# Performance work log

Measured on AMD Instinct MI355X. Metric: run time of the kernel, lower is better.

Reference implementation:

```python
import jax, jax.numpy as jnp
import numpy as np

B, C, H, W = 64, 3, 512, 512
KSIZE = 13
EPS = 8.0
IDENTITY_OFFSET = 4.0
DEFORM_OFFSET = (2.0 + IDENTITY_OFFSET / (W - 1)) / 2.0
SCALE_X = IDENTITY_OFFSET / (W - 1)
SCALE_Y = IDENTITY_OFFSET / (H - 1)


def setup_inputs() -> dict:
    key = jax.random.key(0)
    k1, k2 = jax.random.split(key)
    image = jax.random.uniform(k1, (B, C, H, W), dtype=jnp.float32)
    prim_grid = jax.random.normal(k2, (B, 2, H, W), dtype=jnp.float32) * 0.01
    return {"image": image, "prim_grid": prim_grid}


def _samp_iden():
    seq = jnp.arange(-(W - 1), W, 2, dtype=jnp.float32) / (W - 1)
    gx = jnp.broadcast_to(seq[None, :], (H, W))
    gy = gx.T
    return jnp.stack([gx, gy], axis=0)[None]  # [1,2,H,W]


def _gaussian_blur(x, ksize):
    sigma = ksize * 0.15 + 0.35
    half = (ksize - 1) * 0.5
    t = jnp.linspace(-half, half, ksize)
    pdf = jnp.exp(-0.5 * (t / sigma) ** 2)
    k1 = pdf / pdf.sum()
    k2d = jnp.outer(k1, k1)
    p = ksize // 2
    xp = jnp.pad(x, ((0, 0), (0, 0), (p, p), (p, p)), mode='reflect')
    kernel = jnp.broadcast_to(k2d[None, None], (2, 1, ksize, ksize))
    return jax.lax.conv_general_dilated(
        xp, kernel, window_strides=(1, 1), padding='VALID',
        feature_group_count=2, dimension_numbers=('NCHW', 'OIHW', 'NCHW'))


def _samp2accu(samp):
    # conv_transpose with [1,-1] kernel + crop == first-difference with zero prepend
    s = samp + DEFORM_OFFSET
    ax = jnp.diff(s[:, 0:1], axis=3, prepend=jnp.zeros_like(s[:, 0:1, :, :1])) / SCALE_X
    ay = jnp.diff(s[:, 1:2], axis=2, prepend=jnp.zeros_like(s[:, 1:2, :1, :])) / SCALE_Y
    return jnp.concatenate([ax, ay], axis=1)


def _accu2samp(accu):
    # conv_transpose with full-ones kernel + crop == cumulative sum
    sx = jnp.cumsum(accu[:, 0:1] * SCALE_X, axis=3)
    sy = jnp.cumsum(accu[:, 1:2] * SCALE_Y, axis=2)
    return jnp.concatenate([sx, sy], axis=1) - DEFORM_OFFSET


def _grid_sample(image, grid):
    # image [B,C,H,W], grid [B,H,W,2] xy in [-1,1], bilinear, align_corners=True, zeros pad
    gx = (grid[..., 0] + 1.0) * 0.5 * (W - 1)
    gy = (grid[..., 1] + 1.0) * 0.5 * (H - 1)
    x0 = jnp.floor(gx)
    y0 = jnp.floor(gy)
    wx = gx - x0
    wy = gy - y0
    x0i = x0.astype(jnp.int32)
    x1i = x0i + 1
    y0i = y0.astype(jnp.int32)
    y1i = y0i + 1

    def gather(img, yi, xi):
        valid = ((xi >= 0) & (xi < W) & (yi >= 0) & (yi < H)).astype(img.dtype)
        xc = jnp.clip(xi, 0, W - 1)
        yc = jnp.clip(yi, 0, H - 1)
        return img[:, yc, xc] * valid[None]  # [C,H,W]

    def per_b(img, y0i, y1i, x0i, x1i, wx, wy):
        v00 = gather(img, y0i, x0i)
        v01 = gather(img, y0i, x1i)
        v10 = gather(img, y1i, x0i)
        v11 = gather(img, y1i, x1i)
        return (v00 * (1 - wx) * (1 - wy) + v01 * wx * (1 - wy)
                + v10 * (1 - wx) * wy + v11 * wx * wy)

    return jax.vmap(per_b)(image, y0i, y1i, x0i, x1i, wx, wy)


def _forward_grid(prim_grid):
    iden = _samp_iden()
    p = _gaussian_blur(prim_grid, KSIZE)
    accu = jnp.maximum(_samp2accu(p + iden), 0.0)          # accu_clip (relu)
    p = _accu2samp(accu) - iden
    bound = (2.0 / W) * EPS
    p = jnp.clip(p, -bound, bound)                          # prim_clip
    samp = jnp.clip(p + iden, -1.0, 1.0)                    # samp_clip (hardtanh)
    return samp


def reference(image, prim_grid):
    samp = _forward_grid(prim_grid)
    grid = jnp.transpose(samp, (0, 2, 3, 1))  # [B,H,W,2]
    return _grid_sample(image, grid)
```

## Files before the change

kernel.cpp:

```cpp
#include <hip/hip_runtime.h>
#include <math.h>

#define HH 512
#define WW 512
#define NB 64
#define HW (HH*WW)

struct GaussK { float k[13]; };

__device__ __forceinline__ float idenv(int i) {
    return (float)(2*i - (WW-1)) / (float)(WW-1);
}

#define DEF_OFF ((float)((2.0 + 4.0/511.0)/2.0))
#define BOUND   ((float)(2.0/512.0*8.0))

typedef float vf2 __attribute__((ext_vector_type(2), aligned(4)));

__device__ __forceinline__ void hconv_row(const float (&a)[8], int lane, const GaussK& gk, float (&o)[8]) {
    float win[20];
    #pragma unroll
    for (int i = 0; i < 6; ++i) {
        float v = __shfl_up(a[i+2], 1, 64);
        win[i] = (lane == 0) ? a[6-i] : v;
    }
    #pragma unroll
    for (int i = 6; i < 14; ++i) win[i] = a[i-6];
    #pragma unroll
    for (int i = 14; i < 20; ++i) {
        float v = __shfl_down(a[i-14], 1, 64);
        win[i] = (lane == 63) ? a[20-i] : v;
    }
    #pragma unroll
    for (int j = 0; j < 8; ++j) {
        float acc = 0.f;
        #pragma unroll
        for (int i = 0; i < 13; ++i) acc = fmaf(gk.k[i], win[j+i], acc);
        o[j] = acc;
    }
}

__device__ __forceinline__ void xscan_row(const float (&a)[8], int lane, const GaussK& gk, float* row0) {
    float win[21];
    #pragma unroll
    for (int i = 0; i < 7; ++i) {
        float v = __shfl_up(a[i+1], 1, 64);
        win[i] = (lane == 0) ? a[7-i] : v;
    }
    #pragma unroll
    for (int i = 0; i < 8; ++i) win[7+i] = a[i];
    #pragma unroll
    for (int i = 15; i < 21; ++i) {
        float v = __shfl_down(a[i-15], 1, 64);
        win[i] = (lane == 63) ? a[21-i] : v;
    }
    float s[9];
    #pragma unroll
    for (int j = 0; j < 9; ++j) {
        float acc = 0.f;
        #pragma unroll
        for (int i = 0; i < 13; ++i) acc = fmaf(gk.k[i], win[j+i], acc);
        s[j] = acc + idenv(8*lane - 1 + j) + DEF_OFF;
    }
    if (lane == 0) s[0] = 0.f;

    float qs[8], q = 0.f;
    #pragma unroll
    for (int j = 1; j < 9; ++j) { q += fmaxf(s[j] - s[j-1], 0.f); qs[j-1] = q; }
    float inc = q;
    #pragma unroll
    for (int d = 1; d < 64; d <<= 1) {
        float t = __shfl_up(inc, d, 64);
        if (lane >= d) inc += t;
    }
    float excl = inc - q;

    float4 g0, g1;
    float* gp0 = (float*)&g0;
    float* gp1 = (float*)&g1;
    #pragma unroll
    for (int j = 0; j < 8; ++j) {
        int wcol = lane*8 + j;
        float sx = excl + qs[j];
        float p = sx - DEF_OFF - idenv(wcol);
        p = fminf(fmaxf(p, -BOUND), BOUND);
        float g = p + idenv(wcol);
        g = fminf(fmaxf(g, -1.f), 1.f);
        if (j < 4) gp0[j] = g; else gp1[j-4] = g;
    }
    *(float4*)(row0 + lane*8)     = g0;
    *(float4*)(row0 + lane*8 + 4) = g1;
}

__global__ void __launch_bounds__(256) k_prep(const float* __restrict__ prim, float* __restrict__ out, GaussK gk) {
    int lane = threadIdx.x & 63;
    int bid  = (int)blockIdx.x;
    int work = (bid & 7)*256 + (bid >> 3);
    int gw   = work*4 + ((int)threadIdx.x >> 6);
    int b    = gw >> 7;
    int h0   = (gw & 127)*4;

    const float4* src0 = (const float4*)(prim + (size_t)b*2*HW);
    const float*  src1 = prim + ((size_t)b*2 + 1)*HW;
    float* plane0 = out + (size_t)b*3*HW;
    float* plane1 = out + ((size_t)b*3 + 1)*HW;

    float a[4][8];
    #pragma unroll
    for (int r = 0; r < 4; ++r)
        #pragma unroll
        for (int j = 0; j < 8; ++j) a[r][j] = 0.f;

    #pragma unroll
    for (int i = 0; i < 16; ++i) {
        int rr = h0 - 6 + i;
        rr = rr < 0 ? -rr : (rr > HH-1 ? 2*(HH-1) - rr : rr);
        float4 u0 = src0[(size_t)rr*128 + 2*lane];
        float4 u1 = src0[(size_t)rr*128 + 2*lane + 1];
        float vv[8] = {u0.x,u0.y,u0.z,u0.w,u1.x,u1.y,u1.z,u1.w};
        #pragma unroll
        for (int r = 0; r < 4; ++r) {
            if (i >= r && i <= r + 12) {
                #pragma unroll
                for (int j = 0; j < 8; ++j) a[r][j] = fmaf(gk.k[i-r], vv[j], a[r][j]);
            }
        }
    }

    #pragma unroll
    for (int r = 0; r < 4; ++r) {
        const float4* c4 = (const float4*)(src1 + (size_t)(h0+r)*WW);
        float4 u0 = c4[2*lane];
        float4 u1 = c4[2*lane + 1];
        float c[8] = {u0.x,u0.y,u0.z,u0.w,u1.x,u1.y,u1.z,u1.w};
        float o[8];
        hconv_row(c, lane, gk, o);
        float* row1 = plane1 + (size_t)(h0+r)*WW;
        *(float4*)(row1 + lane*8)     = make_float4(o[0],o[1],o[2],o[3]);
        *(float4*)(row1 + lane*8 + 4) = make_float4(o[4],o[5],o[6],o[7]);
    }

    #pragma unroll
    for (int r = 0; r < 4; ++r)
        xscan_row(a[r], lane, gk, plane0 + (size_t)(h0+r)*WW);
}

__global__ void __launch_bounds__(1024, 1) k_yssamp(const float* __restrict__ image, float* __restrict__ out, GaussK gk) {
    __shared__ float segsum[16][64];
    int bid  = (int)blockIdx.x;
    int work = (bid & 7)*64 + (bid >> 3);
    int b    = work >> 3;
    int wt   = work & 7;
    int lane = threadIdx.x & 63;
    int ws   = threadIdx.x >> 6;
    int w    = wt*64 + lane;
    const float* p1 = out + ((size_t)b*3 + 1)*HW + w;
    int r0 = ws*32;

    float v[45];
    #pragma unroll
    for (int j = 0; j < 45; ++j) {
        int r = r0 - 7 + j;
        r = r < 0 ? -r : (r > HH-1 ? 2*(HH-1) - r : r);
        v[j] = p1[(size_t)r*WW];
    }

    float sprev;
    if (ws == 0) {
        sprev = 0.f;
    } else {
        float acc = 0.f;
        #pragma unroll
        for (int i = 0; i < 13; ++i) acc = fmaf(gk.k[i], v[i], acc);
        sprev = acc + idenv(r0 - 1) + DEF_OFF;
    }

    float q[32];
    float run = 0.f;
    #pragma unroll
    for (int n = 0; n < 32; ++n) {
        float acc = 0.f;
        #pragma unroll
        for (int i = 0; i < 13; ++i) acc = fmaf(gk.k[i], v[n+1+i], acc);
        float s = acc + idenv(r0 + n) + DEF_OFF;
        run += fmaxf(s - sprev, 0.f);
        q[n] = run;
        sprev = s;
    }
    segsum[ws][lane] = run;
    __syncthreads();
    float off = 0.f;
    for (int k = 0; k < ws; ++k) off += segsum[k][lane];

    const float* ib = image + (size_t)b*3*HW;
    float*       ob = out   + (size_t)b*3*HW;

    float gxv[32];
    #pragma unroll
    for (int n = 0; n < 32; ++n)
        gxv[n] = ob[(size_t)(r0 + n)*WW + w];

    #pragma unroll
    for (int n = 0; n < 32; ++n) {
        int h = r0 + n;
        size_t poff = (size_t)h*WW + w;
        float p = off + q[n] - DEF_OFF - idenv(h);
        p = fminf(fmaxf(p, -BOUND), BOUND);
        float gy = p + idenv(h);
        gy = fminf(fmaxf(gy, -1.f), 1.f);
        float gx = gxv[n];

        float fx = (gx + 1.f) * 0.5f * (float)(WW-1);
        float fy = (gy + 1.f) * 0.5f * (float)(HH-1);
        float x0f = floorf(fx), y0f = floorf(fy);
        float wx = fx - x0f, wy = fy - y0f;
        int x0 = (int)x0f, y0 = (int)y0f;
        int y1 = y0 + 1; if (y1 > HH-1) y1 = HH-1;
        bool shx = x0 > WW-2;
        int xb = shx ? WW-2 : x0;
        size_t g0 = (size_t)y0*WW + xb;
        size_t g1 = (size_t)y1*WW + xb;
        float w11 = wx*wy;
        float w01 = wx - w11;
        float w10 = wy - w11;
        float w00 = 1.f - wx - wy + w11;
        #pragma unroll
        for (int c = 0; c < 3; ++c) {
            const float* ip = ib + (size_t)c*HW;
            vf2 t  = *(const vf2*)(ip + g0);
            vf2 bo = *(const vf2*)(ip + g1);
            float a00 = shx ? t.y  : t.x;
            float a10 = shx ? bo.y : bo.x;
            float r = a00*w00 + t.y*w01 + a10*w10 + bo.y*w11;
            __builtin_nontemporal_store(r, ob + (size_t)c*HW + poff);
        }
    }
}

extern "C" void kernel_launch(void* const* d_in, const int* in_sizes, int n_in,
                              void* d_out, int out_size, void* d_ws, size_t ws_size,
                              hipStream_t stream) {
    const float* image = (const float*)d_in[0];
    const float* prim  = (const float*)d_in[1];
    float* out = (float*)d_out;

    GaussK gk;
    {
        double sigma = 13.0*0.15 + 0.35;
        double pdf[13], sum = 0.0;
        for (int i = 0; i < 13; ++i) {
            double t = (double)(i - 6);
            pdf[i] = exp(-0.5*(t/sigma)*(t/sigma));
            sum += pdf[i];
        }
        for (int i = 0; i < 13; ++i) gk.k[i] = (float)(pdf[i]/sum);
    }

    k_prep  <<<2048, 256,  0, stream>>>(prim, out, gk);
    k_yssamp<<<NB*8, 1024, 0, stream>>>(image, out, gk);
}
```

Measured before the change: 226.0 us.

## Stage image tiles in shared memory for bilinear sampling in y-scan kernel

The y-scan kernel now writes the y sampling coordinate to the third output plane. Then, for each 64x64 output tile, it cooperatively loads an 80x80 halo tile of all three image channels into LDS and does the bilinear gathers from LDS instead of from global memory. This relies on displacements staying within the ±8-pixel halo, which the prim clip bound guarantees. The cost is an extra global write and read of the gy plane, about 77KB of LDS per block, and two barriers per tile.

```diff
diff --git a/kernel.cpp b/kernel.cpp
--- a/kernel.cpp
+++ b/kernel.cpp
@@ -145,95 +145,131 @@
         xscan_row(a[r], lane, gk, plane0 + (size_t)(h0+r)*WW);
 }
 
-__global__ void __launch_bounds__(1024, 1) k_yssamp(const float* __restrict__ image, float* __restrict__ out, GaussK gk) {
+__global__ void __launch_bounds__(1024) k_yssamp(const float* __restrict__ image, float* __restrict__ out, GaussK gk) {
     __shared__ float segsum[16][64];
+    __shared__ float img[3][80][80];
     int bid  = (int)blockIdx.x;
-    int work = (bid & 7)*64 + (bid >> 3);
-    int b    = work >> 3;
-    int wt   = work & 7;
+    int b    = bid >> 3;
+    int wt   = bid & 7;
+    int c0   = wt*64;
     int lane = threadIdx.x & 63;
     int ws   = threadIdx.x >> 6;
-    int w    = wt*64 + lane;
+    int w    = c0 + lane;
     const float* p1 = out + ((size_t)b*3 + 1)*HW + w;
+    float*       p2 = out + ((size_t)b*3 + 2)*HW + w;
     int r0 = ws*32;
 
-    float v[45];
-    #pragma unroll
-    for (int j = 0; j < 45; ++j) {
-        int r = r0 - 7 + j;
-        r = r < 0 ? -r : (r > HH-1 ? 2*(HH-1) - r : r);
-        v[j] = p1[(size_t)r*WW];
-    }
-
-    float sprev;
-    if (ws == 0) {
-        sprev = 0.f;
-    } else {
-        float acc = 0.f;
-        #pragma unroll
-        for (int i = 0; i < 13; ++i) acc = fmaf(gk.k[i], v[i], acc);
-        sprev = acc + idenv(r0 - 1) + DEF_OFF;
-    }
-
-    float q[32];
-    float run = 0.f;
-    #pragma unroll
-    for (int n = 0; n < 32; ++n) {
-        float acc = 0.f;
-        #pragma unroll
-        for (int i = 0; i < 13; ++i) acc = fmaf(gk.k[i], v[n+1+i], acc);
-        float s = acc + idenv(r0 + n) + DEF_OFF;
-        run += fmaxf(s - sprev, 0.f);
-        q[n] = run;
-        sprev = s;
-    }
-    segsum[ws][lane] = run;
+    {
+        float v[45];
+        #pragma unroll
+        for (int j = 0; j < 45; ++j) {
+            int r = r0 - 7 + j;
+            r = r < 0 ? -r : (r > HH-1 ? 2*(HH-1) - r : r);
+            v[j] = p1[(size_t)r*WW];
+        }
+        float sprev;
+        if (ws == 0) {
+            sprev = 0.f;
+        } else {
+            float acc = 0.f;
+            #pragma unroll
+            for (int i = 0; i < 13; ++i) acc = fmaf(gk.k[i], v[i], acc);
+            sprev = acc + idenv(r0 - 1) + DEF_OFF;
+        }
+        float q[32];
+        float run = 0.f;
+        #pragma unroll
+        for (int n = 0; n < 32; ++n) {
+            float acc = 0.f;
+            #pragma unroll
+            for (int i = 0; i < 13; ++i) acc = fmaf(gk.k[i], v[n+1+i], acc);
+            float s = acc + idenv(r0 + n) + DEF_OFF;
+            run += fmaxf(s - sprev, 0.f);
+            q[n] = run;
+            sprev = s;
+        }
+        segsum[ws][lane] = run;
+        __syncthreads();
+        float off = 0.f;
+        for (int k = 0; k < ws; ++k) off += segsum[k][lane];
+        #pragma unroll
+        for (int n = 0; n < 32; ++n) {
+            int h = r0 + n;
+            float p = off + q[n] - DEF_OFF - idenv(h);
+            p = fminf(fmaxf(p, -BOUND), BOUND);
+            float g = p + idenv(h);
+            g = fminf(fmaxf(g, -1.f), 1.f);
+            p2[(size_t)h*WW] = g;
+        }
+    }
     __syncthreads();
-    float off = 0.f;
-    for (int k = 0; k < ws; ++k) off += segsum[k][lane];
-
-    const float* ib = image + (size_t)b*3*HW;
-    float*       ob = out   + (size_t)b*3*HW;
-
-    float gxv[32];
-    #pragma unroll
-    for (int n = 0; n < 32; ++n)
-        gxv[n] = ob[(size_t)(r0 + n)*WW + w];
-
-    #pragma unroll
-    for (int n = 0; n < 32; ++n) {
-        int h = r0 + n;
-        size_t poff = (size_t)h*WW + w;
-        float p = off + q[n] - DEF_OFF - idenv(h);
-        p = fminf(fmaxf(p, -BOUND), BOUND);
-        float gy = p + idenv(h);
-        gy = fminf(fmaxf(gy, -1.f), 1.f);
-        float gx = gxv[n];
-
-        float fx = (gx + 1.f) * 0.5f * (float)(WW-1);
-        float fy = (gy + 1.f) * 0.5f * (float)(HH-1);
-        float x0f = floorf(fx), y0f = floorf(fy);
-        float wx = fx - x0f, wy = fy - y0f;
-        int x0 = (int)x0f, y0 = (int)y0f;
-        int y1 = y0 + 1; if (y1 > HH-1) y1 = HH-1;
-        bool shx = x0 > WW-2;
-        int xb = shx ? WW-2 : x0;
-        size_t g0 = (size_t)y0*WW + xb;
-        size_t g1 = (size_t)y1*WW + xb;
-        float w11 = wx*wy;
-        float w01 = wx - w11;
-        float w10 = wy - w11;
-        float w00 = 1.f - wx - wy + w11;
-        #pragma unroll
-        for (int c = 0; c < 3; ++c) {
-            const float* ip = ib + (size_t)c*HW;
-            vf2 t  = *(const vf2*)(ip + g0);
-            vf2 bo = *(const vf2*)(ip + g1);
-            float a00 = shx ? t.y  : t.x;
-            float a10 = shx ? bo.y : bo.x;
-            float r = a00*w00 + t.y*w01 + a10*w10 + bo.y*w11;
-            __builtin_nontemporal_store(r, ob + (size_t)c*HW + poff);
-        }
+
+    const float* ibase = image + (size_t)b*3*HW;
+    float*       obase = out   + (size_t)b*3*HW;
+    int CB  = c0 - 8;
+    int sp  = (int)threadIdx.x >> 2;
+    int sq  = (int)threadIdx.x & 3;
+    int sch = sp / 80;
+    int sri = sp % 80;
+    int lc  = (int)threadIdx.x & 63;
+    int lr0 = ((int)threadIdx.x >> 6) << 2;
+
+    for (int k = 0; k < 8; ++k) {
+        int RB = k*64 - 8;
+        if (sp < 240) {
+            int sr = RB + sri; sr = sr < 0 ? 0 : (sr > HH-1 ? HH-1 : sr);
+            const float* srow = ibase + (size_t)sch*HW + (size_t)sr*WW;
+            #pragma unroll
+            for (int jj = 0; jj < 5; ++jj) {
+                int j  = sq*5 + jj;
+                int sc = CB + 4*j;
+                float4 val;
+                if (sc >= 0 && sc <= WW-4) {
+                    val = *(const float4*)(srow + sc);
+                } else {
+                    int cA = sc;   cA = cA<0?0:(cA>WW-1?WW-1:cA);
+                    int cB = sc+1; cB = cB<0?0:(cB>WW-1?WW-1:cB);
+                    int cC = sc+2; cC = cC<0?0:(cC>WW-1?WW-1:cC);
+                    int cD = sc+3; cD = cD<0?0:(cD>WW-1?WW-1:cD);
+                    val = make_float4(srow[cA], srow[cB], srow[cC], srow[cD]);
+                }
+                *(float4*)&img[sch][sri][4*j] = val;
+            }
+        }
+        __syncthreads();
+
+        #pragma unroll
+        for (int rr = 0; rr < 4; ++rr) {
+            int h = k*64 + lr0 + rr;
+            size_t poff = (size_t)h*WW + c0 + lc;
+            float gx = obase[poff];
+            float gy = obase[2*HW + poff];
+            float fx = (gx + 1.f) * 0.5f * (float)(WW-1);
+            float fy = (gy + 1.f) * 0.5f * (float)(HH-1);
+            float x0f = floorf(fx), y0f = floorf(fy);
+            float wx = fx - x0f, wy = fy - y0f;
+            int x0 = (int)x0f, y0 = (int)y0f;
+            bool shx = x0 > WW-2;
+            int xb = shx ? WW-2 : x0;
+            int tx  = xb - CB;
+            int y1 = y0 + 1; if (y1 > HH-1) y1 = HH-1;
+            int ty0 = y0 - RB;
+            int ty1 = y1 - RB;
+            float w11 = wx*wy;
+            float w01 = wx - w11;
+            float w10 = wy - w11;
+            float w00 = 1.f - wx - wy + w11;
+            #pragma unroll
+            for (int c = 0; c < 3; ++c) {
+                float f00 = img[c][ty0][tx],  f01 = img[c][ty0][tx+1];
+                float f10 = img[c][ty1][tx],  f11 = img[c][ty1][tx+1];
+                float a00 = shx ? f01 : f00;
+                float a10 = shx ? f11 : f10;
+                float r = a00*w00 + f01*w01 + a10*w10 + f11*w11;
+                __builtin_nontemporal_store(r, obase + (size_t)c*HW + poff);
+            }
+        }
+        __syncthreads();
     }
 }
 
```

After: 318.3 us. +40.8%, slower.

## Stage gy grid to output plane and sample two adjacent pixels per thread

Applied to the files above, without the earlier changes.

The y-scan phase now writes its clipped gy grid into the third output plane. After a block barrier, the sampling phase reassigns threads so each one handles two horizontally adjacent pixels over 16 rows. When both samples fall in the same source row at consecutive x positions, it gathers them with a single 4-wide load per channel and stores both results as one 2-wide write. This cuts gather instructions and widens the stores. The cost is an extra round trip of the gy plane through memory, a second barrier, a divergent fallback path, and dropping the min-blocks launch bound.

```diff
diff --git a/kernel.cpp b/kernel.cpp
--- a/kernel.cpp
+++ b/kernel.cpp
@@ -16,6 +16,7 @@
 #define BOUND   ((float)(2.0/512.0*8.0))
 
 typedef float vf2 __attribute__((ext_vector_type(2), aligned(4)));
+typedef float vf4 __attribute__((ext_vector_type(4), aligned(4)));
 
 __device__ __forceinline__ void hconv_row(const float (&a)[8], int lane, const GaussK& gk, float (&o)[8]) {
     float win[20];
@@ -145,94 +146,132 @@
         xscan_row(a[r], lane, gk, plane0 + (size_t)(h0+r)*WW);
 }
 
-__global__ void __launch_bounds__(1024, 1) k_yssamp(const float* __restrict__ image, float* __restrict__ out, GaussK gk) {
+__global__ void __launch_bounds__(1024) k_yssamp(const float* __restrict__ image, float* __restrict__ out, GaussK gk) {
     __shared__ float segsum[16][64];
     int bid  = (int)blockIdx.x;
     int work = (bid & 7)*64 + (bid >> 3);
     int b    = work >> 3;
     int wt   = work & 7;
+    int c0   = wt*64;
     int lane = threadIdx.x & 63;
     int ws   = threadIdx.x >> 6;
-    int w    = wt*64 + lane;
+    int w    = c0 + lane;
     const float* p1 = out + ((size_t)b*3 + 1)*HW + w;
+    float*       p2 = out + ((size_t)b*3 + 2)*HW + w;
     int r0 = ws*32;
 
-    float v[45];
-    #pragma unroll
-    for (int j = 0; j < 45; ++j) {
-        int r = r0 - 7 + j;
-        r = r < 0 ? -r : (r > HH-1 ? 2*(HH-1) - r : r);
-        v[j] = p1[(size_t)r*WW];
-    }
-
-    float sprev;
-    if (ws == 0) {
-        sprev = 0.f;
-    } else {
-        float acc = 0.f;
-        #pragma unroll
-        for (int i = 0; i < 13; ++i) acc = fmaf(gk.k[i], v[i], acc);
-        sprev = acc + idenv(r0 - 1) + DEF_OFF;
-    }
-
-    float q[32];
-    float run = 0.f;
-    #pragma unroll
-    for (int n = 0; n < 32; ++n) {
-        float acc = 0.f;
-        #pragma unroll
-        for (int i = 0; i < 13; ++i) acc = fmaf(gk.k[i], v[n+1+i], acc);
-        float s = acc + idenv(r0 + n) + DEF_OFF;
-        run += fmaxf(s - sprev, 0.f);
-        q[n] = run;
-        sprev = s;
-    }
-    segsum[ws][lane] = run;
+    {
+        float v[45];
+        #pragma unroll
+        for (int j = 0; j < 45; ++j) {
+            int r = r0 - 7 + j;
+            r = r < 0 ? -r : (r > HH-1 ? 2*(HH-1) - r : r);
+            v[j] = p1[(size_t)r*WW];
+        }
+        float sprev;
+        if (ws == 0) {
+            sprev = 0.f;
+        } else {
+            float acc = 0.f;
+            #pragma unroll
+            for (int i = 0; i < 13; ++i) acc = fmaf(gk.k[i], v[i], acc);
+            sprev = acc + idenv(r0 - 1) + DEF_OFF;
+        }
+        float q[32];
+        float run = 0.f;
+        #pragma unroll
+        for (int n = 0; n < 32; ++n) {
+            float acc = 0.f;
+            #pragma unroll
+            for (int i = 0; i < 13; ++i) acc = fmaf(gk.k[i], v[n+1+i], acc);
+            float s = acc + idenv(r0 + n) + DEF_OFF;
+            run += fmaxf(s - sprev, 0.f);
+            q[n] = run;
+            sprev = s;
+        }
+        segsum[ws][lane] = run;
+        __syncthreads();
+        float off = 0.f;
+        for (int k = 0; k < ws; ++k) off += segsum[k][lane];
+        #pragma unroll
+        for (int n = 0; n < 32; ++n) {
+            int h = r0 + n;
+            float p = off + q[n] - DEF_OFF - idenv(h);
+            p = fminf(fmaxf(p, -BOUND), BOUND);
+            float g = p + idenv(h);
+            g = fminf(fmaxf(g, -1.f), 1.f);
+            p2[(size_t)h*WW] = g;
+        }
+    }
     __syncthreads();
-    float off = 0.f;
-    for (int k = 0; k < ws; ++k) off += segsum[k][lane];
 
     const float* ib = image + (size_t)b*3*HW;
     float*       ob = out   + (size_t)b*3*HW;
-
-    float gxv[32];
-    #pragma unroll
-    for (int n = 0; n < 32; ++n)
-        gxv[n] = ob[(size_t)(r0 + n)*WW + w];
-
-    #pragma unroll
-    for (int n = 0; n < 32; ++n) {
-        int h = r0 + n;
-        size_t poff = (size_t)h*WW + w;
-        float p = off + q[n] - DEF_OFF - idenv(h);
-        p = fminf(fmaxf(p, -BOUND), BOUND);
-        float gy = p + idenv(h);
-        gy = fminf(fmaxf(gy, -1.f), 1.f);
-        float gx = gxv[n];
-
-        float fx = (gx + 1.f) * 0.5f * (float)(WW-1);
-        float fy = (gy + 1.f) * 0.5f * (float)(HH-1);
-        float x0f = floorf(fx), y0f = floorf(fy);
-        float wx = fx - x0f, wy = fy - y0f;
-        int x0 = (int)x0f, y0 = (int)y0f;
-        int y1 = y0 + 1; if (y1 > HH-1) y1 = HH-1;
-        bool shx = x0 > WW-2;
-        int xb = shx ? WW-2 : x0;
-        size_t g0 = (size_t)y0*WW + xb;
-        size_t g1 = (size_t)y1*WW + xb;
-        float w11 = wx*wy;
-        float w01 = wx - w11;
-        float w10 = wy - w11;
-        float w00 = 1.f - wx - wy + w11;
+    int tid = (int)threadIdx.x;
+    int cp  = tid & 31;
+    int rg  = tid >> 5;
+    int col = c0 + 2*cp;
+
+    for (int rr = 0; rr < 16; ++rr) {
+        int h = rg*16 + rr;
+        size_t off = (size_t)h*WW + col;
+        vf2 gx2 = *(const vf2*)(ob + off);
+        vf2 gy2 = *(const vf2*)(ob + 2*HW + off);
+
+        float fx0 = (gx2.x + 1.f) * 0.5f * (float)(WW-1);
+        float fx1 = (gx2.y + 1.f) * 0.5f * (float)(WW-1);
+        float fy0 = (gy2.x + 1.f) * 0.5f * (float)(HH-1);
+        float fy1 = (gy2.y + 1.f) * 0.5f * (float)(HH-1);
+        float xf0 = floorf(fx0), xf1 = floorf(fx1);
+        float yf0 = floorf(fy0), yf1 = floorf(fy1);
+        float wx0 = fx0 - xf0, wx1 = fx1 - xf1;
+        float wy0 = fy0 - yf0, wy1 = fy1 - yf1;
+        int x00 = (int)xf0, x01 = (int)xf1;
+        int y00 = (int)yf0, y01 = (int)yf1;
+        bool sh0 = x00 > WW-2, sh1 = x01 > WW-2;
+        int xb0 = sh0 ? WW-2 : x00, xb1 = sh1 ? WW-2 : x01;
+        int y10 = y00 + 1 > HH-1 ? HH-1 : y00 + 1;
+        int y11 = y01 + 1 > HH-1 ? HH-1 : y01 + 1;
+
+        float w110 = wx0*wy0, w010 = wx0 - w110, w100 = wy0 - w110, w000 = 1.f - wx0 - wy0 + w110;
+        float w111 = wx1*wy1, w011 = wx1 - w111, w101 = wy1 - w111, w001 = 1.f - wx1 - wy1 + w111;
+
+        float r0c[3], r1c[3];
+        if (y00 == y01 && xb1 == xb0 + 1 && xb0 <= WW-4) {
+            size_t gt = (size_t)y00*WW + xb0;
+            size_t gb = (size_t)y10*WW + xb0;
+            #pragma unroll
+            for (int c = 0; c < 3; ++c) {
+                const float* ip = ib + (size_t)c*HW;
+                vf4 t  = *(const vf4*)(ip + gt);
+                vf4 bo = *(const vf4*)(ip + gb);
+                r0c[c] = t.x*w000 + t.y*w010 + bo.x*w100 + bo.y*w110;
+                r1c[c] = t.y*w001 + t.z*w011 + bo.y*w101 + bo.z*w111;
+            }
+        } else {
+            size_t g00 = (size_t)y00*WW + xb0, g10 = (size_t)y10*WW + xb0;
+            size_t g01 = (size_t)y01*WW + xb1, g11 = (size_t)y11*WW + xb1;
+            #pragma unroll
+            for (int c = 0; c < 3; ++c) {
+                const float* ip = ib + (size_t)c*HW;
+                vf2 t0 = *(const vf2*)(ip + g00);
+                vf2 b0 = *(const vf2*)(ip + g10);
+                vf2 t1 = *(const vf2*)(ip + g01);
+                vf2 b1 = *(const vf2*)(ip + g11);
+                float a000 = sh0 ? t0.y : t0.x;
+                float a100 = sh0 ? b0.y : b0.x;
+                r0c[c] = a000*w000 + t0.y*w010 + a100*w100 + b0.y*w110;
+                float a001 = sh1 ? t1.y : t1.x;
+                float a101 = sh1 ? b1.y : b1.x;
+                r1c[c] = a001*w001 + t1.y*w011 + a101*w101 + b1.y*w111;
+            }
+        }
         #pragma unroll
         for (int c = 0; c < 3; ++c) {
-            const float* ip = ib + (size_t)c*HW;
-            vf2 t  = *(const vf2*)(ip + g0);
-            vf2 bo = *(const vf2*)(ip + g1);
-            float a00 = shx ? t.y  : t.x;
-            float a10 = shx ? bo.y : bo.x;
-            float r = a00*w00 + t.y*w01 + a10*w10 + bo.y*w11;
-            __builtin_nontemporal_store(r, ob + (size_t)c*HW + poff);
+            vf2 rv;
+            rv.x = r0c[c];
+            rv.y = r1c[c];
+            __builtin_nontemporal_store(rv, (vf2*)(ob + (size_t)c*HW + off));
         }
     }
 }
```

After: 318.1 us. +40.8%, slower.
